# Kernel tuning notes

Measured on AMD Instinct MI355X. Metric: run time of the kernel, lower is better.

Reference implementation:

```python
import jax, jax.numpy as jnp
import numpy as np

N, E, D, L = 50000, 625000, 128, 7
EPS = 1e-7   # GENConv message epsilon
T = 1.0      # softmax aggregation temperature (learn_t=False)
NUM_ATOM_FEATS, ATOM_VOCAB = 9, 64
NUM_BOND_FEATS, BOND_VOCAB = 3, 8


def setup_inputs() -> dict:
    key = jax.random.key(0)
    ks = jax.random.split(key, 9)
    x = jax.random.randint(ks[0], (N, NUM_ATOM_FEATS), 0, ATOM_VOCAB, dtype=jnp.int32)
    edge_index = jax.random.randint(ks[1], (2, E), 0, N, dtype=jnp.int32)
    edge_attr = jax.random.randint(ks[2], (E, NUM_BOND_FEATS), 0, BOND_VOCAB, dtype=jnp.int32)
    atom_emb = jax.random.normal(ks[3], (NUM_ATOM_FEATS, ATOM_VOCAB, D), dtype=jnp.float32) * 0.1
    bond_emb = jax.random.normal(ks[4], (NUM_BOND_FEATS, BOND_VOCAB, D), dtype=jnp.float32) * 0.1
    W = jax.random.normal(ks[5], (L, D, D), dtype=jnp.float32) / np.sqrt(D).astype(np.float32)
    b = jnp.zeros((L, D), dtype=jnp.float32)
    ln_gamma = jnp.ones((L, D), dtype=jnp.float32)
    ln_beta = jnp.zeros((L, D), dtype=jnp.float32)
    return dict(x=x, edge_index=edge_index, edge_attr=edge_attr,
                atom_emb=atom_emb, bond_emb=bond_emb, W=W, b=b,
                ln_gamma=ln_gamma, ln_beta=ln_beta)


def _layer_norm(h, g, bta):
    mu = jnp.mean(h, axis=-1, keepdims=True)
    var = jnp.var(h, axis=-1, keepdims=True)
    return (h - mu) * jax.lax.rsqrt(var + 1e-5) * g + bta


def _gen_conv(h, src, dst, edge_emb, Wl, bl):
    # GENConv: msg = relu(x_j + e) + eps; softmax aggregation over dst; Linear(x + m)
    msg = jax.nn.relu(h[src] + edge_emb) + EPS                 # [E, D]
    logits = msg * T
    seg_max = jax.ops.segment_max(logits, dst, num_segments=N)  # [N, D]
    seg_max = jnp.where(jnp.isfinite(seg_max), seg_max, 0.0)    # empty segments
    e = jnp.exp(logits - seg_max[dst])                          # [E, D]
    denom = jax.ops.segment_sum(e, dst, num_segments=N)         # [N, D]
    alpha = e / (denom[dst] + 1e-16)
    m = jax.ops.segment_sum(alpha * msg, dst, num_segments=N)   # [N, D]
    return (h + m) @ Wl + bl


def reference(x, edge_index, edge_attr, atom_emb, bond_emb, W, b, ln_gamma, ln_beta):
    src, dst = edge_index[0], edge_index[1]
    # AtomEncoder: sum of per-feature embedding lookups -> [N, D]
    h = jnp.sum(atom_emb[jnp.arange(NUM_ATOM_FEATS)[None, :], x], axis=1)
    # BondEncoder (conv_encode_edge=False: encoded once) -> [E, D]
    edge_emb = jnp.sum(bond_emb[jnp.arange(NUM_BOND_FEATS)[None, :], edge_attr], axis=1)
    # res+ block, dropout=0 (no-op)
    h = _gen_conv(h, src, dst, edge_emb, W[0], b[0])
    for layer in range(1, L):
        h2 = jax.nn.relu(_layer_norm(h, ln_gamma[layer - 1], ln_beta[layer - 1]))
        h = _gen_conv(h2, src, dst, edge_emb, W[layer], b[layer]) + h
    h = _layer_norm(h, ln_gamma[L - 1], ln_beta[L - 1])
    return h
```

## Files before the change

kernel.cpp:

```cpp
#include <hip/hip_runtime.h>
#include <hip/hip_fp16.h>
#include <math.h>


constexpr int D = 128;
constexpr int NA = 9;
constexpr int NB = 3;
constexpr float L2E = 1.4426950408889634f;
constexpr float INV_L2E = 0.6931471805599453f;

using half8  = __attribute__((ext_vector_type(8))) _Float16;
using h2v    = __attribute__((ext_vector_type(2))) _Float16;
using floatx4 = __attribute__((ext_vector_type(4))) float;


__global__ void k_hist(const int* __restrict__ dst, int* __restrict__ deg, int E) {
    int e = blockIdx.x * 256 + threadIdx.x;
    if (e < E) atomicAdd(&deg[dst[e]], 1);
}

__global__ void k_scan_a(const int* __restrict__ deg, int* __restrict__ offs,
                         int* __restrict__ bsum, int N) {
    __shared__ int s[256];
    int i = blockIdx.x * 256 + threadIdx.x;
    int v = (i < N) ? deg[i] : 0;
    s[threadIdx.x] = v;
    __syncthreads();
    for (int d = 1; d < 256; d <<= 1) {
        int add = (threadIdx.x >= d) ? s[threadIdx.x - d] : 0;
        __syncthreads();
        s[threadIdx.x] += add;
        __syncthreads();
    }
    if (i < N) offs[i + 1] = s[threadIdx.x];
    if (threadIdx.x == 255) bsum[blockIdx.x] = s[255];
    if (i == 0) offs[0] = 0;
}

__global__ void k_scan_b(const int* __restrict__ bsum, int* __restrict__ bexc, int nb) {
    __shared__ int s[256];
    int t = threadIdx.x;
    int v = (t < nb) ? bsum[t] : 0;
    s[t] = v;
    __syncthreads();
    for (int d = 1; d < 256; d <<= 1) {
        int add = (t >= d) ? s[t - d] : 0;
        __syncthreads();
        s[t] += add;
        __syncthreads();
    }
    if (t < nb) bexc[t] = s[t] - v;
}

__global__ void k_scan_c(int* __restrict__ offs, const int* __restrict__ bexc, int N) {
    int i = blockIdx.x * 256 + threadIdx.x;
    if (i < N) offs[i + 1] += bexc[blockIdx.x];
}

__global__ void k_fill(const int* __restrict__ src, const int* __restrict__ dst,
                       const int* __restrict__ attr, const int* __restrict__ offs,
                       int* __restrict__ cur, int2* __restrict__ recs, int E) {
    int e = blockIdx.x * 256 + threadIdx.x;
    if (e >= E) return;
    int d = dst[e];
    int pos = offs[d] + atomicAdd(&cur[d], 1);
    int cidx = attr[e * 3] * 64 + attr[e * 3 + 1] * 8 + attr[e * 3 + 2];
    recs[pos] = make_int2(src[e], cidx);
}


__global__ void k_dhist(const int* __restrict__ deg, int* __restrict__ dbin, int N) {
    __shared__ int lb[64];
    int t = threadIdx.x;
    if (t < 64) lb[t] = 0;
    __syncthreads();
    int i = blockIdx.x * 256 + t;
    if (i < N) {
        int d = deg[i]; d = d < 63 ? d : 63;
        atomicAdd(&lb[63 - d], 1);
    }
    __syncthreads();
    if (t < 64 && lb[t] > 0) atomicAdd(&dbin[t], lb[t]);
}

__global__ void k_dscan(const int* __restrict__ dbin, int* __restrict__ doff) {
    if (threadIdx.x == 0) {
        int acc = 0;
        for (int b = 0; b < 64; ++b) { doff[b] = acc; acc += dbin[b]; }
    }
}

__global__ void k_dfill(const int* __restrict__ deg, const int* __restrict__ doff,
                        int* __restrict__ dcur, int* __restrict__ perm, int N) {
    __shared__ int lc[64], lbase[64];
    int t = threadIdx.x;
    if (t < 64) lc[t] = 0;
    __syncthreads();
    int i = blockIdx.x * 256 + t;
    int b = 0, rank = 0;
    if (i < N) {
        int d = deg[i]; d = d < 63 ? d : 63;
        b = 63 - d;
        rank = atomicAdd(&lc[b], 1);
    }
    __syncthreads();
    if (t < 64 && lc[t] > 0) lbase[t] = atomicAdd(&dcur[t], lc[t]);
    __syncthreads();
    if (i < N) perm[doff[b] + lbase[b] + rank] = i;
}

__global__ void k_comb(const float* __restrict__ bemb, __half* __restrict__ comb16) {
    int gid = blockIdx.x * 256 + threadIdx.x;
    int c = gid >> 5, q = gid & 31;
    int a0 = c >> 6, a1 = (c >> 3) & 7, a2 = c & 7;
    float4 v0 = *(const float4*)(bemb + (a0)*D + q * 4);
    float4 v1 = *(const float4*)(bemb + (8 + a1) * D + q * 4);
    float4 v2 = *(const float4*)(bemb + (16 + a2) * D + q * 4);
    __half2* c2 = (__half2*)comb16;
    c2[c * 64 + q * 2]     = __floats2half2_rn(L2E * (v0.x + v1.x + v2.x),
                                               L2E * (v0.y + v1.y + v2.y));
    c2[c * 64 + q * 2 + 1] = __floats2half2_rn(L2E * (v0.z + v1.z + v2.z),
                                               L2E * (v0.w + v1.w + v2.w));
}

__global__ void k_wt(const float* __restrict__ W, __half* __restrict__ Wt16, int total) {
    int o = blockIdx.x * 256 + threadIdx.x;
    if (o >= total) return;
    int l = o >> 14;
    int rem = o & 16383;
    int f = rem >> 7, k = rem & 127;
    Wt16[o] = __float2half_rn(W[(l << 14) + k * 128 + f]);
}


__global__ void k_atom(const int* __restrict__ x, const float* __restrict__ aemb,
                       __half* __restrict__ h16, int N) {
    int wid = (blockIdx.x * blockDim.x + threadIdx.x) >> 6;
    int lane = threadIdx.x & 63;
    if (wid >= N) return;
    const int* xr = x + wid * NA;
    float ax = 0.f, ay = 0.f;
#pragma unroll
    for (int f = 0; f < NA; ++f) {
        int v = xr[f];
        const float2 e = *(const float2*)(aemb + (f * 64 + v) * D + 2 * lane);
        ax += e.x; ay += e.y;
    }
    ((__half2*)h16)[wid * 64 + lane] = __floats2half2_rn(ax * L2E, ay * L2E);
}


__global__ __launch_bounds__(256) void k_agg(const __half* __restrict__ h16,
                      const int2* __restrict__ recs,
                      const int* __restrict__ offs, const __half* __restrict__ comb16,
                      const int* __restrict__ perm,
                      __half* __restrict__ t16, int N) {
    int wid = (blockIdx.x * blockDim.x + threadIdx.x) >> 6;
    int lane = threadIdx.x & 63;
    if (wid >= N) return;
    int nid = perm[wid];
    int su = __builtin_amdgcn_readfirstlane(offs[nid]);
    int eu = __builtin_amdgcn_readfirstlane(offs[nid + 1]);
    h2v hm2 = ((const h2v*)h16)[nid * 64 + lane];
    float hsx = (float)hm2[0], hsy = (float)hm2[1];
    if (su >= eu) {
        ((__half2*)t16)[nid * 64 + lane] =
            __floats2half2_rn(hsx * INV_L2E, hsy * INV_L2E);
        return;
    }
    float Sx = 0.f, Sy = 0.f, Wx = 0.f, Wy = 0.f;
    int last = eu - 1;

    const h2v* hrow = (const h2v*)h16 + lane;
    const h2v* crow = (const h2v*)comb16 + lane;

    const h2v zero2 = (h2v)(_Float16)0;
    const h2v eps2  = {(_Float16)(1e-7f * L2E), (_Float16)(1e-7f * L2E)};

    h2v hq[16], cq[16];

    auto load4 = [&](int base, int slot) {
#pragma unroll
        for (int i = 0; i < 4; ++i) {
            int idx = base + i; idx = (idx < last) ? idx : last;
            int2 rr = recs[idx];
            int sj = __builtin_amdgcn_readfirstlane(rr.x);
            int cj = __builtin_amdgcn_readfirstlane(rr.y);
            hq[slot * 4 + i] = hrow[sj * 64];
            cq[slot * 4 + i] = crow[cj * 64];
        }
    };
    auto comp4u = [&](int slot) {
#pragma unroll
        for (int i = 0; i < 4; ++i) {
            h2v m = hq[slot * 4 + i] + cq[slot * 4 + i];
            m = __builtin_elementwise_max(m, zero2);
            m = m + eps2;
            float u0 = (float)m[0], u1 = (float)m[1];
            float px = __builtin_amdgcn_exp2f(u0);
            float py = __builtin_amdgcn_exp2f(u1);
            Sx += px; Sy += py;
            Wx = fmaf(px, u0, Wx);
            Wy = fmaf(py, u1, Wy);
        }
    };
    auto comp4m = [&](int gb, int slot) {
#pragma unroll
        for (int i = 0; i < 4; ++i) {
            h2v m = hq[slot * 4 + i] + cq[slot * 4 + i];
            m = __builtin_elementwise_max(m, zero2);
            m = m + eps2;
            float u0 = (float)m[0], u1 = (float)m[1];
            bool valid = (gb + i) < eu;
            float px = valid ? __builtin_amdgcn_exp2f(u0) : 0.f;
            float py = valid ? __builtin_amdgcn_exp2f(u1) : 0.f;
            Sx += px; Sy += py;
            Wx = fmaf(px, u0, Wx);
            Wy = fmaf(py, u1, Wy);
        }
    };

    load4(su, 0);
    if (su + 4  < eu) load4(su + 4, 1);
    if (su + 8  < eu) load4(su + 8, 2);
    if (su + 12 < eu) load4(su + 12, 3);

    int e = su;
    for (; e + 16 < eu; e += 16) {
        comp4u(0); comp4u(1); comp4u(2); comp4u(3);
        load4(e + 16, 0); load4(e + 20, 1); load4(e + 24, 2); load4(e + 28, 3);
    }
    comp4m(e, 0);
    if (e + 4  < eu) comp4m(e + 4, 1);
    if (e + 8  < eu) comp4m(e + 8, 2);
    if (e + 12 < eu) comp4m(e + 12, 3);

    float tx = (hsx + Wx / (Sx + 1e-16f)) * INV_L2E;
    float ty = (hsy + Wy / (Sy + 1e-16f)) * INV_L2E;
    ((__half2*)t16)[nid * 64 + lane] = __floats2half2_rn(tx, ty);
}


template <int MODE>
__global__ __launch_bounds__(256) void k_gemm(const __half* __restrict__ A16,
                                              const __half* __restrict__ Wt16,
                                              const float* __restrict__ bl,
                                              const __half* __restrict__ res16,
                                              __half* __restrict__ hres16,
                                              const float* __restrict__ g,
                                              const float* __restrict__ bta,
                                              __half* __restrict__ h16,
                                              float* __restrict__ out,
                                              int N, int useRes) {
    int lane = threadIdx.x & 63;
    int wave = threadIdx.x >> 6;
    int quad = lane >> 4, col = lane & 15;
    int node = blockIdx.x * 64 + wave * 16 + col;
    bool nok = node < N;
    int nc = nok ? node : N - 1;

    const __half* arow = A16 + (size_t)nc * 128;
    half8 bfrag[4];
#pragma unroll
    for (int ks = 0; ks < 4; ++ks)
        bfrag[ks] = *(const half8*)(arow + ks * 32 + quad * 8);

    floatx4 acc[8];
#pragma unroll
    for (int ft = 0; ft < 8; ++ft) acc[ft] = (floatx4){0.f, 0.f, 0.f, 0.f};

#pragma unroll
    for (int ft = 0; ft < 8; ++ft) {
        const __half* wrow = Wt16 + (size_t)(ft * 16 + col) * 128;
#pragma unroll
        for (int ks = 0; ks < 4; ++ks) {
            half8 afrag = *(const half8*)(wrow + ks * 32 + quad * 8);
            acc[ft] = __builtin_amdgcn_mfma_f32_16x16x32_f16(afrag, bfrag[ks],
                                                             acc[ft], 0, 0, 0);
        }
    }

    float s = 0.f, ss = 0.f;
#pragma unroll
    for (int ft = 0; ft < 8; ++ft) {
        int f0 = ft * 16 + quad * 4;
        float4 bb = *(const float4*)(bl + f0);
        float o0 = acc[ft][0] + bb.x, o1 = acc[ft][1] + bb.y;
        float o2 = acc[ft][2] + bb.z, o3 = acc[ft][3] + bb.w;
        if (useRes) {
            uint2 rr = *(const uint2*)(res16 + (size_t)nc * 128 + f0);
            __half2 r01 = *(__half2*)&rr.x, r23 = *(__half2*)&rr.y;
            o0 += __low2float(r01); o1 += __high2float(r01);
            o2 += __low2float(r23); o3 += __high2float(r23);
        }
        acc[ft][0] = o0; acc[ft][1] = o1; acc[ft][2] = o2; acc[ft][3] = o3;
        s += (o0 + o1) + (o2 + o3);
        ss += fmaf(o0, o0, o1 * o1) + fmaf(o2, o2, o3 * o3);
        if (MODE == 0 && nok) {
            __half2 h01 = __floats2half2_rn(o0, o1);
            __half2 h23 = __floats2half2_rn(o2, o3);
            uint2 pk = make_uint2(*(unsigned*)&h01, *(unsigned*)&h23);
            *(uint2*)(hres16 + (size_t)node * 128 + f0) = pk;
        }
    }
    s += __shfl_xor(s, 16, 64);  ss += __shfl_xor(ss, 16, 64);
    s += __shfl_xor(s, 32, 64);  ss += __shfl_xor(ss, 32, 64);
    float mu = s * (1.f / 128.f);
    float var = ss * (1.f / 128.f) - mu * mu;
    float rs = rsqrtf(var + 1e-5f);

#pragma unroll
    for (int ft = 0; ft < 8; ++ft) {
        int f0 = ft * 16 + quad * 4;
        float4 gg = *(const float4*)(g + f0);
        float4 bt = *(const float4*)(bta + f0);
        float l0 = (acc[ft][0] - mu) * rs * gg.x + bt.x;
        float l1 = (acc[ft][1] - mu) * rs * gg.y + bt.y;
        float l2 = (acc[ft][2] - mu) * rs * gg.z + bt.z;
        float l3 = (acc[ft][3] - mu) * rs * gg.w + bt.w;
        if (MODE == 0) {
            l0 = fmaxf(l0, 0.f); l1 = fmaxf(l1, 0.f);
            l2 = fmaxf(l2, 0.f); l3 = fmaxf(l3, 0.f);
            if (nok) {
                __half2 h01 = __floats2half2_rn(l0 * L2E, l1 * L2E);
                __half2 h23 = __floats2half2_rn(l2 * L2E, l3 * L2E);
                uint2 pk = make_uint2(*(unsigned*)&h01, *(unsigned*)&h23);
                *(uint2*)(h16 + (size_t)node * 128 + f0) = pk;
            }
        } else {
            if (nok)
                *(float4*)(out + (size_t)node * 128 + f0) =
                    make_float4(l0, l1, l2, l3);
        }
    }
}


extern "C" void kernel_launch(void* const* d_in, const int* in_sizes, int n_in,
                              void* d_out, int out_size, void* d_ws, size_t ws_size,
                              hipStream_t stream) {
    const int*   x    = (const int*)d_in[0];
    const int*   ei   = (const int*)d_in[1];
    const int*   attr = (const int*)d_in[2];
    const float* aemb = (const float*)d_in[3];
    const float* bemb = (const float*)d_in[4];
    const float* Wf   = (const float*)d_in[5];
    const float* bf   = (const float*)d_in[6];
    const float* gam  = (const float*)d_in[7];
    const float* bet  = (const float*)d_in[8];
    float* out = (float*)d_out;

    const int N = in_sizes[0] / NA;
    const int E = in_sizes[1] / 2;
    const int L = in_sizes[5] / (D * D);

    char* ws = (char*)d_ws;
    size_t o = 0;
    auto carve = [&](size_t bytes) -> void* {
        void* p = (void*)(ws + o);
        o += (bytes + 255) & ~(size_t)255;
        return p;
    };
    __half* hres16 = (__half*)carve((size_t)N * D * 2);
    __half* h16    = (__half*)carve((size_t)N * D * 2);
    __half* t16    = (__half*)carve((size_t)N * D * 2);
    int2*   recs   = (int2*)carve((size_t)E * 8);
    __half* comb16 = (__half*)carve(512 * D * 2);
    __half* Wt16   = (__half*)carve((size_t)L * D * D * 2);
    int*    deg    = (int*)carve((size_t)N * 4);
    int*    cur    = (int*)carve((size_t)N * 4);
    int*    offs   = (int*)carve((size_t)(N + 1) * 4);
    int*    perm   = (int*)carve((size_t)N * 4);
    int*    dbin   = (int*)carve(256);
    int*    doff   = (int*)carve(256);
    int*    dcur   = (int*)carve(256);
    int*    bsum   = (int*)carve(4096);
    int*    bexc   = (int*)carve(4096);

    const int* src = ei;
    const int* dst = ei + E;

    hipMemsetAsync(deg, 0, (size_t)N * 4, stream);
    hipMemsetAsync(cur, 0, (size_t)N * 4, stream);
    hipMemsetAsync(dbin, 0, 256, stream);
    hipMemsetAsync(dcur, 0, 256, stream);

    int ebl = (E + 255) / 256;
    int nbl = (N + 255) / 256;
    k_comb<<<64, 256, 0, stream>>>(bemb, comb16);
    int wtot = L * D * D;
    k_wt<<<(wtot + 255) / 256, 256, 0, stream>>>(Wf, Wt16, wtot);
    k_hist<<<ebl, 256, 0, stream>>>(dst, deg, E);
    k_scan_a<<<nbl, 256, 0, stream>>>(deg, offs, bsum, N);
    k_scan_b<<<1, 256, 0, stream>>>(bsum, bexc, nbl);
    k_scan_c<<<nbl, 256, 0, stream>>>(offs, bexc, N);
    k_fill<<<ebl, 256, 0, stream>>>(src, dst, attr, offs, cur, recs, E);
    k_dhist<<<nbl, 256, 0, stream>>>(deg, dbin, N);
    k_dscan<<<1, 64, 0, stream>>>(dbin, doff);
    k_dfill<<<nbl, 256, 0, stream>>>(deg, doff, dcur, perm, N);

    int wbl = (N * 64 + 255) / 256;
    k_atom<<<wbl, 256, 0, stream>>>(x, aemb, h16, N);

    int gbl = (N + 63) / 64;
    for (int l = 0; l < L; ++l) {
        k_agg<<<wbl, 256, 0, stream>>>(h16, recs, offs, comb16, perm, t16, N);
        if (l == L - 1) {
            k_gemm<1><<<gbl, 256, 0, stream>>>(t16, Wt16 + l * D * D, bf + l * D,
                                               hres16, hres16,
                                               gam + l * D, bet + l * D, h16, out,
                                               N, 1);
        } else {
            k_gemm<0><<<gbl, 256, 0, stream>>>(t16, Wt16 + l * D * D, bf + l * D,
                                               hres16, hres16,
                                               gam + l * D, bet + l * D, h16, out,
                                               N, l > 0 ? 1 : 0);
        }
    }
}
```

Before: 618.3 us.

## Split wave into four edge groups with 16-byte half8 gathers in aggregation

The aggregation kernel now splits each 64-lane wave into four groups of 16 lanes. Each group handles a different edge, and each lane loads 8 halves with one 16-byte vector gather instead of one half2 per lane across all 64 lanes. The per-group partial sums and weighted sums are combined with cross-lane shuffles at the end, and the 16 lanes of group 0 write the result. This cuts the number of gather instructions and per-edge register queues, but adds shuffle reductions, keeps 8 accumulators per lane, and lets lanes in one wave diverge on edge indices (no readfirstlane).

```diff
diff --git a/kernel.cpp b/kernel.cpp
--- a/kernel.cpp
+++ b/kernel.cpp
@@ -158,65 +158,70 @@
     int wid = (blockIdx.x * blockDim.x + threadIdx.x) >> 6;
     int lane = threadIdx.x & 63;
     if (wid >= N) return;
+    int g = lane >> 4;
+    int s = lane & 15;
     int nid = perm[wid];
     int su = __builtin_amdgcn_readfirstlane(offs[nid]);
     int eu = __builtin_amdgcn_readfirstlane(offs[nid + 1]);
-    h2v hm2 = ((const h2v*)h16)[nid * 64 + lane];
-    float hsx = (float)hm2[0], hsy = (float)hm2[1];
+
+    half8 hs8 = ((const half8*)h16)[nid * 16 + s];
+
     if (su >= eu) {
-        ((__half2*)t16)[nid * 64 + lane] =
-            __floats2half2_rn(hsx * INV_L2E, hsy * INV_L2E);
+        if (g == 0) {
+            __half2 a = __floats2half2_rn((float)hs8[0] * INV_L2E, (float)hs8[1] * INV_L2E);
+            __half2 b = __floats2half2_rn((float)hs8[2] * INV_L2E, (float)hs8[3] * INV_L2E);
+            __half2 c = __floats2half2_rn((float)hs8[4] * INV_L2E, (float)hs8[5] * INV_L2E);
+            __half2 d = __floats2half2_rn((float)hs8[6] * INV_L2E, (float)hs8[7] * INV_L2E);
+            uint4 pk = make_uint4(*(unsigned*)&a, *(unsigned*)&b,
+                                  *(unsigned*)&c, *(unsigned*)&d);
+            *(uint4*)(t16 + (size_t)nid * 128 + s * 8) = pk;
+        }
         return;
     }
-    float Sx = 0.f, Sy = 0.f, Wx = 0.f, Wy = 0.f;
+
+    float S[8], Wc[8];
+#pragma unroll
+    for (int i = 0; i < 8; ++i) { S[i] = 0.f; Wc[i] = 0.f; }
     int last = eu - 1;
 
-    const h2v* hrow = (const h2v*)h16 + lane;
-    const h2v* crow = (const h2v*)comb16 + lane;
-
-    const h2v zero2 = (h2v)(_Float16)0;
-    const h2v eps2  = {(_Float16)(1e-7f * L2E), (_Float16)(1e-7f * L2E)};
-
-    h2v hq[16], cq[16];
+    const half8* hbase = (const half8*)h16 + s;
+    const half8* cbase = (const half8*)comb16 + s;
+
+    const half8 zero8 = (half8)(_Float16)0;
+    const _Float16 epse = (_Float16)(1e-7f * L2E);
+    const half8 eps8 = {epse, epse, epse, epse, epse, epse, epse, epse};
+
+    half8 hq[4], cq[4];
 
     auto load4 = [&](int base, int slot) {
-#pragma unroll
-        for (int i = 0; i < 4; ++i) {
-            int idx = base + i; idx = (idx < last) ? idx : last;
-            int2 rr = recs[idx];
-            int sj = __builtin_amdgcn_readfirstlane(rr.x);
-            int cj = __builtin_amdgcn_readfirstlane(rr.y);
-            hq[slot * 4 + i] = hrow[sj * 64];
-            cq[slot * 4 + i] = crow[cj * 64];
-        }
+        int idx = base + g; idx = (idx < last) ? idx : last;
+        int2 rr = recs[idx];
+        hq[slot] = hbase[rr.x * 16];
+        cq[slot] = cbase[rr.y * 16];
     };
     auto comp4u = [&](int slot) {
-#pragma unroll
-        for (int i = 0; i < 4; ++i) {
-            h2v m = hq[slot * 4 + i] + cq[slot * 4 + i];
-            m = __builtin_elementwise_max(m, zero2);
-            m = m + eps2;
-            float u0 = (float)m[0], u1 = (float)m[1];
-            float px = __builtin_amdgcn_exp2f(u0);
-            float py = __builtin_amdgcn_exp2f(u1);
-            Sx += px; Sy += py;
-            Wx = fmaf(px, u0, Wx);
-            Wy = fmaf(py, u1, Wy);
+        half8 m = hq[slot] + cq[slot];
+        m = __builtin_elementwise_max(m, zero8);
+        m = m + eps8;
+#pragma unroll
+        for (int i = 0; i < 8; ++i) {
+            float u = (float)m[i];
+            float p = __builtin_amdgcn_exp2f(u);
+            S[i] += p;
+            Wc[i] = fmaf(p, u, Wc[i]);
         }
     };
     auto comp4m = [&](int gb, int slot) {
-#pragma unroll
-        for (int i = 0; i < 4; ++i) {
-            h2v m = hq[slot * 4 + i] + cq[slot * 4 + i];
-            m = __builtin_elementwise_max(m, zero2);
-            m = m + eps2;
-            float u0 = (float)m[0], u1 = (float)m[1];
-            bool valid = (gb + i) < eu;
-            float px = valid ? __builtin_amdgcn_exp2f(u0) : 0.f;
-            float py = valid ? __builtin_amdgcn_exp2f(u1) : 0.f;
-            Sx += px; Sy += py;
-            Wx = fmaf(px, u0, Wx);
-            Wy = fmaf(py, u1, Wy);
+        half8 m = hq[slot] + cq[slot];
+        m = __builtin_elementwise_max(m, zero8);
+        m = m + eps8;
+        bool valid = (gb + g) < eu;
+#pragma unroll
+        for (int i = 0; i < 8; ++i) {
+            float u = (float)m[i];
+            float p = valid ? __builtin_amdgcn_exp2f(u) : 0.f;
+            S[i] += p;
+            Wc[i] = fmaf(p, u, Wc[i]);
         }
     };
 
@@ -235,9 +240,27 @@
     if (e + 8  < eu) comp4m(e + 8, 2);
     if (e + 12 < eu) comp4m(e + 12, 3);
 
-    float tx = (hsx + Wx / (Sx + 1e-16f)) * INV_L2E;
-    float ty = (hsy + Wy / (Sy + 1e-16f)) * INV_L2E;
-    ((__half2*)t16)[nid * 64 + lane] = __floats2half2_rn(tx, ty);
+#pragma unroll
+    for (int i = 0; i < 8; ++i) {
+        S[i]  += __shfl_xor(S[i], 16, 64);
+        S[i]  += __shfl_xor(S[i], 32, 64);
+        Wc[i] += __shfl_xor(Wc[i], 16, 64);
+        Wc[i] += __shfl_xor(Wc[i], 32, 64);
+    }
+
+    if (g == 0) {
+        float t[8];
+#pragma unroll
+        for (int i = 0; i < 8; ++i)
+            t[i] = ((float)hs8[i] + Wc[i] / (S[i] + 1e-16f)) * INV_L2E;
+        __half2 a = __floats2half2_rn(t[0], t[1]);
+        __half2 b = __floats2half2_rn(t[2], t[3]);
+        __half2 c = __floats2half2_rn(t[4], t[5]);
+        __half2 d = __floats2half2_rn(t[6], t[7]);
+        uint4 pk = make_uint4(*(unsigned*)&a, *(unsigned*)&b,
+                              *(unsigned*)&c, *(unsigned*)&d);
+        *(uint4*)(t16 + (size_t)nid * 128 + s * 8) = pk;
+    }
 }
 
 
```

New measurement: 707.1 us. +14.4%, slower.
